# Performance work log

Hardware: AMD Instinct MI355X
Metric: run time of the kernel (lower is better)

## Reference

```python
import jax, jax.numpy as jnp
import numpy as np

B, NNODE, FIN, FOUT = 64, 512, 64, 64

def setup_inputs() -> dict:
    key = jax.random.key(0)
    ks = jax.random.split(key, 8)
    stdW = 1.0 / np.sqrt(FIN)
    stdA = 1.0 / np.sqrt(FOUT)
    return {
        "X": jax.random.normal(ks[0], (B, NNODE, FIN), dtype=jnp.float32),
        "A": jax.random.uniform(ks[1], (B, NNODE, NNODE), dtype=jnp.float32),
        "N": jax.random.randint(ks[2], (B,), 1, NNODE + 1, dtype=jnp.int64),
        "W": jax.random.uniform(ks[3], (FIN, FOUT), jnp.float32, -stdW, stdW),
        "a": jax.random.uniform(ks[4], (FOUT, FOUT), jnp.float32, -stdA, stdA),
        "bias_W": jax.random.uniform(ks[5], (FOUT,), jnp.float32, -stdW, stdW),
        "bias_a": jax.random.uniform(ks[6], (NNODE,), jnp.float32, -1.0 / np.sqrt(NNODE), 1.0 / np.sqrt(NNODE)),
    }

def reference(X, A, N, W, a, bias_W, bias_a):
    # A_ = A + identity on the top-left n_atoms block (only diagonal entries)
    idx = jnp.arange(A.shape[1])
    diag_mask = (idx[None, :] < N[:, None]).astype(A.dtype)  # [B, n]
    A_ = A + jnp.einsum('bn,nm->bnm', diag_mask, jnp.eye(A.shape[1], dtype=A.dtype))
    # XW: [B, n, F_out]
    XW = jnp.einsum('bnc,cd->bnd', X, W)
    # buf[a,j,k] = sum_i a[i,j] * XW^T[a,j,k]  (einsum 'ij,ajk->ajk')
    col_sum = a.sum(axis=0)  # [F_out]
    XWT = jnp.swapaxes(XW, 1, 2)  # [B, F_out, n]
    buf = col_sum[None, :, None] * XWT
    Z = jnp.einsum('bif,bfk->bik', XW, buf) + bias_a  # [B, n, n] + [n] broadcast on last dim
    att = jnp.tanh(jnp.einsum('bij,bjk->bik', A_, Z))
    H = jnp.einsum('bij,bjd->bid', att, XW) + bias_W
    return H
```

## Files before the change

### kernel.cpp

```cpp
#include <hip/hip_runtime.h>

#define BB 64
#define NN 512
#define FD 64

typedef short bf16x8 __attribute__((ext_vector_type(8)));
typedef float f32x4 __attribute__((ext_vector_type(4)));

__device__ __forceinline__ unsigned short f2bf(float f){
    unsigned u = __builtin_bit_cast(unsigned, f);
    u += 0x7fffu + ((u >> 16) & 1u);
    return (unsigned short)(u >> 16);
}
__device__ __forceinline__ float bf2f(unsigned short h){
    unsigned u = ((unsigned)h) << 16;
    return __builtin_bit_cast(float, u);
}
__device__ __forceinline__ float fast_tanh(float x){
    float e = __expf(2.0f * x);
    return 1.0f - 2.0f * __builtin_amdgcn_rcpf(e + 1.0f);
}

__global__ __launch_bounds__(256) void k_prep(const float* __restrict__ W,
                                              const float* __restrict__ a,
                                              float* __restrict__ colsum,
                                              unsigned short* __restrict__ Wt){
    int t = threadIdx.x;
    if (t < 64){
        float s = 0.f;
        #pragma unroll
        for (int i = 0; i < 64; i++) s += a[i*64 + t];
        colsum[t] = s;
    }
    int e0 = t * 16;
    int d = e0 >> 6, c0 = e0 & 63;
    #pragma unroll
    for (int q = 0; q < 16; q++)
        Wt[e0 + q] = f2bf(W[(c0 + q)*64 + d]);
}

__global__ __launch_bounds__(256) void k_xw(const float* __restrict__ X,
                                            const unsigned short* __restrict__ Wt,
                                            const float* __restrict__ colsum,
                                            unsigned short* __restrict__ XWh,
                                            unsigned short* __restrict__ XWt,
                                            unsigned short* __restrict__ St){
    __shared__ unsigned short Xl[64][72];
    __shared__ unsigned short Wtl[64][72];
    __shared__ unsigned short Cl[64][72];
    __shared__ float csl[64];
    int t = threadIdx.x;
    int row0 = blockIdx.x * 64;
    int r = t >> 2, c0 = (t & 3) * 16;
    {
        const float4* src = (const float4*)&X[(row0 + r)*FD + c0];
        #pragma unroll
        for (int q = 0; q < 4; q++){
            float4 v = src[q];
            ushort4 h; h.x=f2bf(v.x); h.y=f2bf(v.y); h.z=f2bf(v.z); h.w=f2bf(v.w);
            *(ushort4*)&Xl[r][c0 + q*4] = h;
        }
    }
    {
        const uint4* src = (const uint4*)&Wt[r*64 + c0];
        *(uint4*)&Wtl[r][c0]     = src[0];
        *(uint4*)&Wtl[r][c0 + 8] = src[1];
    }
    if (t < 64) csl[t] = colsum[t];
    __syncthreads();

    int lane = t & 63, w = t >> 6, l15 = lane & 15, quad = lane >> 4;
    f32x4 acc[4] = {{0,0,0,0},{0,0,0,0},{0,0,0,0},{0,0,0,0}};
    #pragma unroll
    for (int ks = 0; ks < 2; ks++){
        bf16x8 af = *(const bf16x8*)&Xl[w*16 + l15][ks*32 + quad*8];
        #pragma unroll
        for (int nt = 0; nt < 4; nt++){
            bf16x8 bfr = *(const bf16x8*)&Wtl[nt*16 + l15][ks*32 + quad*8];
            acc[nt] = __builtin_amdgcn_mfma_f32_16x16x32_bf16(af, bfr, acc[nt], 0, 0, 0);
        }
    }
    #pragma unroll
    for (int nt = 0; nt < 4; nt++)
        #pragma unroll
        for (int rg = 0; rg < 4; rg++)
            Cl[w*16 + quad*4 + rg][nt*16 + l15] = f2bf(acc[nt][rg]);
    __syncthreads();
    {
        uint4 v0 = *(const uint4*)&Cl[r][c0];
        uint4 v1 = *(const uint4*)&Cl[r][c0 + 8];
        *(uint4*)&XWh[(row0 + r)*FD + c0]     = v0;
        *(uint4*)&XWh[(row0 + r)*FD + c0 + 8] = v1;
    }
    {
        int b = blockIdx.x >> 3;
        int n0 = (blockIdx.x & 7) * 64;
        int f = r;
        float cs = csl[f];
        ushort4 hv[4], sv[4];
        #pragma unroll
        for (int q = 0; q < 4; q++)
            #pragma unroll
            for (int jj = 0; jj < 4; jj++){
                unsigned short hb = Cl[c0 + q*4 + jj][f];
                ((unsigned short*)&hv[q])[jj] = hb;
                ((unsigned short*)&sv[q])[jj] = f2bf(bf2f(hb) * cs);
            }
        unsigned short* dstT = &XWt[(b*64 + f)*NN + n0 + c0];
        unsigned short* dstS = &St [(b*64 + f)*NN + n0 + c0];
        #pragma unroll
        for (int q = 0; q < 4; q++){
            *(ushort4*)&dstT[q*4] = hv[q];
            *(ushort4*)&dstS[q*4] = sv[q];
        }
    }
}

__global__ __launch_bounds__(256) void k_m(const float* __restrict__ A,
                                           const unsigned short* __restrict__ St,
                                           const int* __restrict__ Ni,
                                           unsigned short* __restrict__ Mh,
                                           float* __restrict__ rowsum){
    __shared__ unsigned short Al[64][72];
    __shared__ unsigned short Sl[64][72];
    __shared__ float rsl[64][4];
    int t = threadIdx.x;
    int b = blockIdx.y, it = blockIdx.x;
    int i0 = it * 64;
    int Nb = (Ni[1] == 0) ? Ni[2*b] : Ni[b];
    int r = t >> 2, c0 = (t & 3) * 16;
    int lane = t & 63, w = t >> 6, l15 = lane & 15, quad = lane >> 4;
    f32x4 acc[4] = {{0,0,0,0},{0,0,0,0},{0,0,0,0},{0,0,0,0}};
    float rs = 0.f;
    const float* Ab = A + (b*NN + i0)*NN;
    for (int c = 0; c < 8; c++){
        __syncthreads();
        const float4* src = (const float4*)&Ab[r*NN + c*64 + c0];
        #pragma unroll
        for (int q = 0; q < 4; q++){
            float4 v = src[q];
            rs += v.x + v.y + v.z + v.w;
            ushort4 h; h.x=f2bf(v.x); h.y=f2bf(v.y); h.z=f2bf(v.z); h.w=f2bf(v.w);
            *(ushort4*)&Al[r][c0 + q*4] = h;
        }
        const uint4* s2 = (const uint4*)&St[(b*64 + r)*NN + c*64 + c0];
        *(uint4*)&Sl[r][c0]     = s2[0];
        *(uint4*)&Sl[r][c0 + 8] = s2[1];
        __syncthreads();
        #pragma unroll
        for (int ks = 0; ks < 2; ks++){
            bf16x8 af = *(const bf16x8*)&Al[w*16 + l15][ks*32 + quad*8];
            #pragma unroll
            for (int nt = 0; nt < 4; nt++){
                bf16x8 bfr = *(const bf16x8*)&Sl[nt*16 + l15][ks*32 + quad*8];
                acc[nt] = __builtin_amdgcn_mfma_f32_16x16x32_bf16(af, bfr, acc[nt], 0, 0, 0);
            }
        }
        if (c == it){
            #pragma unroll
            for (int nt = 0; nt < 4; nt++)
                #pragma unroll
                for (int rg = 0; rg < 4; rg++){
                    int iloc = w*16 + quad*4 + rg;
                    if (i0 + iloc < Nb)
                        acc[nt][rg] += bf2f(Sl[nt*16 + l15][iloc]);
                }
        }
    }
    rsl[r][t & 3] = rs;
    __syncthreads();
    #pragma unroll
    for (int nt = 0; nt < 4; nt++)
        #pragma unroll
        for (int rg = 0; rg < 4; rg++)
            Al[w*16 + quad*4 + rg][nt*16 + l15] = f2bf(acc[nt][rg]);
    __syncthreads();
    {
        uint4 v0 = *(const uint4*)&Al[r][c0];
        uint4 v1 = *(const uint4*)&Al[r][c0 + 8];
        *(uint4*)&Mh[(b*NN + i0 + r)*FD + c0]     = v0;
        *(uint4*)&Mh[(b*NN + i0 + r)*FD + c0 + 8] = v1;
    }
    if (t < 64){
        float s = rsl[t][0] + rsl[t][1] + rsl[t][2] + rsl[t][3];
        if (i0 + t < Nb) s += 1.f;
        rowsum[b*NN + i0 + t] = s;
    }
}

__global__ __launch_bounds__(256) void k_att(const unsigned short* __restrict__ Mh,
                                             const float* __restrict__ rowsum,
                                             const unsigned short* __restrict__ XWh,
                                             const unsigned short* __restrict__ XWt,
                                             const float* __restrict__ bias_a,
                                             const float* __restrict__ bias_W,
                                             float* __restrict__ H){
    __shared__ unsigned short Ml[64][72];
    __shared__ unsigned short Pl[64][72];
    __shared__ unsigned short XWl[64][72];
    __shared__ unsigned short XWtl[64][72];
    __shared__ float rsl[64];
    __shared__ float bl[64];
    int t = threadIdx.x;
    int b = blockIdx.y, it = blockIdx.x;
    int i0 = it * 64;
    int r = t >> 2, c0 = (t & 3) * 16;
    int lane = t & 63, w = t >> 6, l15 = lane & 15, quad = lane >> 4;
    {
        const uint4* src = (const uint4*)&Mh[(b*NN + i0 + r)*FD + c0];
        *(uint4*)&Ml[r][c0]     = src[0];
        *(uint4*)&Ml[r][c0 + 8] = src[1];
    }
    if (t < 64) rsl[t] = rowsum[b*NN + i0 + t];
    __syncthreads();
    bf16x8 maf[2];
    maf[0] = *(const bf16x8*)&Ml[w*16 + l15][quad*8];
    maf[1] = *(const bf16x8*)&Ml[w*16 + l15][32 + quad*8];
    float rs_r[4];
    #pragma unroll
    for (int rg = 0; rg < 4; rg++) rs_r[rg] = rsl[w*16 + quad*4 + rg];
    f32x4 hacc[4] = {{0,0,0,0},{0,0,0,0},{0,0,0,0},{0,0,0,0}};
    for (int jt = 0; jt < 8; jt++){
        __syncthreads();
        const uint4* s1 = (const uint4*)&XWh[(b*NN + jt*64 + r)*FD + c0];
        *(uint4*)&XWl[r][c0]     = s1[0];
        *(uint4*)&XWl[r][c0 + 8] = s1[1];
        const uint4* s2 = (const uint4*)&XWt[(b*64 + r)*NN + jt*64 + c0];
        *(uint4*)&XWtl[r][c0]     = s2[0];
        *(uint4*)&XWtl[r][c0 + 8] = s2[1];
        if (t < 64) bl[t] = bias_a[jt*64 + t];
        __syncthreads();
        #pragma unroll
        for (int nt = 0; nt < 4; nt++){
            float bv = bl[nt*16 + l15];
            f32x4 arg = { rs_r[0]*bv, rs_r[1]*bv, rs_r[2]*bv, rs_r[3]*bv };
            #pragma unroll
            for (int ks = 0; ks < 2; ks++){
                bf16x8 bfr = *(const bf16x8*)&XWl[nt*16 + l15][ks*32 + quad*8];
                arg = __builtin_amdgcn_mfma_f32_16x16x32_bf16(maf[ks], bfr, arg, 0, 0, 0);
            }
            #pragma unroll
            for (int rg = 0; rg < 4; rg++)
                Pl[w*16 + quad*4 + rg][nt*16 + l15] = f2bf(fast_tanh(arg[rg]));
        }
        __syncthreads();
        #pragma unroll
        for (int ks = 0; ks < 2; ks++){
            bf16x8 paf = *(const bf16x8*)&Pl[w*16 + l15][ks*32 + quad*8];
            #pragma unroll
            for (int dt = 0; dt < 4; dt++){
                bf16x8 bfr = *(const bf16x8*)&XWtl[dt*16 + l15][ks*32 + quad*8];
                hacc[dt] = __builtin_amdgcn_mfma_f32_16x16x32_bf16(paf, bfr, hacc[dt], 0, 0, 0);
            }
        }
    }
    #pragma unroll
    for (int dt = 0; dt < 4; dt++){
        float bw = bias_W[dt*16 + l15];
        #pragma unroll
        for (int rg = 0; rg < 4; rg++)
            H[(b*NN + i0 + w*16 + quad*4 + rg)*FD + dt*16 + l15] = hacc[dt][rg] + bw;
    }
}

extern "C" void kernel_launch(void* const* d_in, const int* in_sizes, int n_in,
                              void* d_out, int out_size, void* d_ws, size_t ws_size,
                              hipStream_t stream){
    const float* X      = (const float*)d_in[0];
    const float* A      = (const float*)d_in[1];
    const int*   N      = (const int*)  d_in[2];
    const float* W      = (const float*)d_in[3];
    const float* a      = (const float*)d_in[4];
    const float* bias_W = (const float*)d_in[5];
    const float* bias_a = (const float*)d_in[6];
    float* H = (float*)d_out;
    char* ws = (char*)d_ws;

    unsigned short* XWh = (unsigned short*)(ws);
    unsigned short* XWt = (unsigned short*)(ws + (4u<<20));
    unsigned short* St  = (unsigned short*)(ws + (8u<<20));
    unsigned short* Mh  = (unsigned short*)(ws + (12u<<20));
    float*          rowsum = (float*)(ws + (16u<<20));
    unsigned short* Wt     = (unsigned short*)(ws + (16u<<20) + 131072);
    float*          colsum = (float*)(ws + (16u<<20) + 139264);

    k_prep<<<1, 256, 0, stream>>>(W, a, colsum, Wt);
    k_xw  <<<BB * NN / 64, 256, 0, stream>>>(X, Wt, colsum, XWh, XWt, St);
    k_m   <<<dim3(8, BB), 256, 0, stream>>>(A, St, N, Mh, rowsum);
    k_att <<<dim3(8, BB), 256, 0, stream>>>(Mh, rowsum, XWh, XWt, bias_a, bias_W, H);
}
```

Measured before the change: 147.1 us.

## Fuse M and attention kernels, drop St buffer, prefetch tiles into registers

Merges the A·S product kernel and the attention kernel into one, so the intermediate M and rowsum stay in shared memory and never go to global memory. The column-sum scaling moves from a separate St buffer onto the M accumulator, which removes one global write and read pass. Both main loops now prefetch the next tile into registers while the current one is computed, and k_prep is parallelised with coalesced loads. The cost is more register and LDS use per block, which may reduce occupancy, and a small rounding change from scaling after the product instead of before.

```diff
diff --git a/kernel.cpp b/kernel.cpp
--- a/kernel.cpp
+++ b/kernel.cpp
@@ -25,30 +25,39 @@
                                               const float* __restrict__ a,
                                               float* __restrict__ colsum,
                                               unsigned short* __restrict__ Wt){
+    __shared__ float Wl[64][68];
+    __shared__ float cpart[4][64];
     int t = threadIdx.x;
-    if (t < 64){
-        float s = 0.f;
-        #pragma unroll
-        for (int i = 0; i < 64; i++) s += a[i*64 + t];
-        colsum[t] = s;
-    }
-    int e0 = t * 16;
-    int d = e0 >> 6, c0 = e0 & 63;
-    #pragma unroll
-    for (int q = 0; q < 16; q++)
-        Wt[e0 + q] = f2bf(W[(c0 + q)*64 + d]);
+    int d = t & 63, part = t >> 6;
+    float s = 0.f;
+    #pragma unroll
+    for (int i = 0; i < 16; i++) s += a[(part*16 + i)*64 + d];
+    cpart[part][d] = s;
+    int r = t >> 2, c0 = (t & 3) * 16;
+    {
+        const float4* src = (const float4*)&W[r*64 + c0];
+        #pragma unroll
+        for (int q = 0; q < 4; q++) *(float4*)&Wl[r][c0 + q*4] = src[q];
+    }
+    __syncthreads();
+    if (part == 0) colsum[d] = cpart[0][d] + cpart[1][d] + cpart[2][d] + cpart[3][d];
+    #pragma unroll
+    for (int q = 0; q < 4; q++){
+        ushort4 o;
+        #pragma unroll
+        for (int jj = 0; jj < 4; jj++)
+            ((unsigned short*)&o)[jj] = f2bf(Wl[c0 + q*4 + jj][r]);
+        *(ushort4*)&Wt[r*64 + c0 + q*4] = o;
+    }
 }
 
 __global__ __launch_bounds__(256) void k_xw(const float* __restrict__ X,
                                             const unsigned short* __restrict__ Wt,
-                                            const float* __restrict__ colsum,
                                             unsigned short* __restrict__ XWh,
-                                            unsigned short* __restrict__ XWt,
-                                            unsigned short* __restrict__ St){
+                                            unsigned short* __restrict__ XWt){
     __shared__ unsigned short Xl[64][72];
     __shared__ unsigned short Wtl[64][72];
     __shared__ unsigned short Cl[64][72];
-    __shared__ float csl[64];
     int t = threadIdx.x;
     int row0 = blockIdx.x * 64;
     int r = t >> 2, c0 = (t & 3) * 16;
@@ -60,15 +69,11 @@
             ushort4 h; h.x=f2bf(v.x); h.y=f2bf(v.y); h.z=f2bf(v.z); h.w=f2bf(v.w);
             *(ushort4*)&Xl[r][c0 + q*4] = h;
         }
-    }
-    {
-        const uint4* src = (const uint4*)&Wt[r*64 + c0];
-        *(uint4*)&Wtl[r][c0]     = src[0];
-        *(uint4*)&Wtl[r][c0 + 8] = src[1];
-    }
-    if (t < 64) csl[t] = colsum[t];
-    __syncthreads();
-
+        const uint4* src2 = (const uint4*)&Wt[r*64 + c0];
+        *(uint4*)&Wtl[r][c0]     = src2[0];
+        *(uint4*)&Wtl[r][c0 + 8] = src2[1];
+    }
+    __syncthreads();
     int lane = t & 63, w = t >> 6, l15 = lane & 15, quad = lane >> 4;
     f32x4 acc[4] = {{0,0,0,0},{0,0,0,0},{0,0,0,0},{0,0,0,0}};
     #pragma unroll
@@ -79,6 +84,14 @@
             bf16x8 bfr = *(const bf16x8*)&Wtl[nt*16 + l15][ks*32 + quad*8];
             acc[nt] = __builtin_amdgcn_mfma_f32_16x16x32_bf16(af, bfr, acc[nt], 0, 0, 0);
         }
+    }
+    int b = blockIdx.x >> 3, n0 = (blockIdx.x & 7) * 64;
+    #pragma unroll
+    for (int nt = 0; nt < 4; nt++){
+        ushort4 hv;
+        #pragma unroll
+        for (int rg = 0; rg < 4; rg++) ((unsigned short*)&hv)[rg] = f2bf(acc[nt][rg]);
+        *(ushort4*)&XWt[(b*64 + nt*16 + l15)*NN + n0 + w*16 + quad*4] = hv;
     }
     #pragma unroll
     for (int nt = 0; nt < 4; nt++)
@@ -92,67 +105,68 @@
         *(uint4*)&XWh[(row0 + r)*FD + c0]     = v0;
         *(uint4*)&XWh[(row0 + r)*FD + c0 + 8] = v1;
     }
-    {
-        int b = blockIdx.x >> 3;
-        int n0 = (blockIdx.x & 7) * 64;
-        int f = r;
-        float cs = csl[f];
-        ushort4 hv[4], sv[4];
-        #pragma unroll
-        for (int q = 0; q < 4; q++)
-            #pragma unroll
-            for (int jj = 0; jj < 4; jj++){
-                unsigned short hb = Cl[c0 + q*4 + jj][f];
-                ((unsigned short*)&hv[q])[jj] = hb;
-                ((unsigned short*)&sv[q])[jj] = f2bf(bf2f(hb) * cs);
-            }
-        unsigned short* dstT = &XWt[(b*64 + f)*NN + n0 + c0];
-        unsigned short* dstS = &St [(b*64 + f)*NN + n0 + c0];
-        #pragma unroll
-        for (int q = 0; q < 4; q++){
-            *(ushort4*)&dstT[q*4] = hv[q];
-            *(ushort4*)&dstS[q*4] = sv[q];
-        }
-    }
-}
-
-__global__ __launch_bounds__(256) void k_m(const float* __restrict__ A,
-                                           const unsigned short* __restrict__ St,
-                                           const int* __restrict__ Ni,
-                                           unsigned short* __restrict__ Mh,
-                                           float* __restrict__ rowsum){
-    __shared__ unsigned short Al[64][72];
-    __shared__ unsigned short Sl[64][72];
-    __shared__ float rsl[64][4];
+}
+
+__global__ __launch_bounds__(256) void k_fused(const float* __restrict__ A,
+                                               const unsigned short* __restrict__ XWh,
+                                               const unsigned short* __restrict__ XWt,
+                                               const float* __restrict__ colsum,
+                                               const int* __restrict__ Ni,
+                                               const float* __restrict__ bias_a,
+                                               const float* __restrict__ bias_W,
+                                               float* __restrict__ H){
+    __shared__ unsigned short s0[64][72];
+    __shared__ unsigned short s1[64][72];
+    __shared__ unsigned short Ml[64][72];
+    __shared__ unsigned short Pl[64][72];
+    __shared__ float rspart[64][4];
+    __shared__ float rsl[64];
+    __shared__ float csl[64];
+    __shared__ float bl[64];
     int t = threadIdx.x;
     int b = blockIdx.y, it = blockIdx.x;
     int i0 = it * 64;
     int Nb = (Ni[1] == 0) ? Ni[2*b] : Ni[b];
     int r = t >> 2, c0 = (t & 3) * 16;
     int lane = t & 63, w = t >> 6, l15 = lane & 15, quad = lane >> 4;
+    if (t < 64) csl[t] = colsum[t];
+    const float* Ab = A + (b*NN + i0)*NN;
+
+    float4 pA[4]; uint4 pB[2];
+    {
+        const float4* src = (const float4*)&Ab[r*NN + c0];
+        #pragma unroll
+        for (int q = 0; q < 4; q++) pA[q] = src[q];
+        const uint4* s2 = (const uint4*)&XWt[(b*64 + r)*NN + c0];
+        pB[0] = s2[0]; pB[1] = s2[1];
+    }
     f32x4 acc[4] = {{0,0,0,0},{0,0,0,0},{0,0,0,0},{0,0,0,0}};
     float rs = 0.f;
-    const float* Ab = A + (b*NN + i0)*NN;
     for (int c = 0; c < 8; c++){
         __syncthreads();
-        const float4* src = (const float4*)&Ab[r*NN + c*64 + c0];
         #pragma unroll
         for (int q = 0; q < 4; q++){
-            float4 v = src[q];
+            float4 v = pA[q];
             rs += v.x + v.y + v.z + v.w;
             ushort4 h; h.x=f2bf(v.x); h.y=f2bf(v.y); h.z=f2bf(v.z); h.w=f2bf(v.w);
-            *(ushort4*)&Al[r][c0 + q*4] = h;
-        }
-        const uint4* s2 = (const uint4*)&St[(b*64 + r)*NN + c*64 + c0];
-        *(uint4*)&Sl[r][c0]     = s2[0];
-        *(uint4*)&Sl[r][c0 + 8] = s2[1];
-        __syncthreads();
+            *(ushort4*)&s0[r][c0 + q*4] = h;
+        }
+        *(uint4*)&s1[r][c0]     = pB[0];
+        *(uint4*)&s1[r][c0 + 8] = pB[1];
+        __syncthreads();
+        if (c < 7){
+            const float4* src = (const float4*)&Ab[r*NN + (c+1)*64 + c0];
+            #pragma unroll
+            for (int q = 0; q < 4; q++) pA[q] = src[q];
+            const uint4* s2 = (const uint4*)&XWt[(b*64 + r)*NN + (c+1)*64 + c0];
+            pB[0] = s2[0]; pB[1] = s2[1];
+        }
         #pragma unroll
         for (int ks = 0; ks < 2; ks++){
-            bf16x8 af = *(const bf16x8*)&Al[w*16 + l15][ks*32 + quad*8];
+            bf16x8 af = *(const bf16x8*)&s0[w*16 + l15][ks*32 + quad*8];
             #pragma unroll
             for (int nt = 0; nt < 4; nt++){
-                bf16x8 bfr = *(const bf16x8*)&Sl[nt*16 + l15][ks*32 + quad*8];
+                bf16x8 bfr = *(const bf16x8*)&s1[nt*16 + l15][ks*32 + quad*8];
                 acc[nt] = __builtin_amdgcn_mfma_f32_16x16x32_bf16(af, bfr, acc[nt], 0, 0, 0);
             }
         }
@@ -163,55 +177,24 @@
                 for (int rg = 0; rg < 4; rg++){
                     int iloc = w*16 + quad*4 + rg;
                     if (i0 + iloc < Nb)
-                        acc[nt][rg] += bf2f(Sl[nt*16 + l15][iloc]);
+                        acc[nt][rg] += bf2f(s1[nt*16 + l15][iloc]);
                 }
         }
     }
-    rsl[r][t & 3] = rs;
-    __syncthreads();
-    #pragma unroll
-    for (int nt = 0; nt < 4; nt++)
+    rspart[r][t & 3] = rs;
+    #pragma unroll
+    for (int nt = 0; nt < 4; nt++){
+        float cs = csl[nt*16 + l15];
         #pragma unroll
         for (int rg = 0; rg < 4; rg++)
-            Al[w*16 + quad*4 + rg][nt*16 + l15] = f2bf(acc[nt][rg]);
-    __syncthreads();
-    {
-        uint4 v0 = *(const uint4*)&Al[r][c0];
-        uint4 v1 = *(const uint4*)&Al[r][c0 + 8];
-        *(uint4*)&Mh[(b*NN + i0 + r)*FD + c0]     = v0;
-        *(uint4*)&Mh[(b*NN + i0 + r)*FD + c0 + 8] = v1;
-    }
+            Ml[w*16 + quad*4 + rg][nt*16 + l15] = f2bf(acc[nt][rg] * cs);
+    }
+    __syncthreads();
     if (t < 64){
-        float s = rsl[t][0] + rsl[t][1] + rsl[t][2] + rsl[t][3];
+        float s = rspart[t][0] + rspart[t][1] + rspart[t][2] + rspart[t][3];
         if (i0 + t < Nb) s += 1.f;
-        rowsum[b*NN + i0 + t] = s;
-    }
-}
-
-__global__ __launch_bounds__(256) void k_att(const unsigned short* __restrict__ Mh,
-                                             const float* __restrict__ rowsum,
-                                             const unsigned short* __restrict__ XWh,
-                                             const unsigned short* __restrict__ XWt,
-                                             const float* __restrict__ bias_a,
-                                             const float* __restrict__ bias_W,
-                                             float* __restrict__ H){
-    __shared__ unsigned short Ml[64][72];
-    __shared__ unsigned short Pl[64][72];
-    __shared__ unsigned short XWl[64][72];
-    __shared__ unsigned short XWtl[64][72];
-    __shared__ float rsl[64];
-    __shared__ float bl[64];
-    int t = threadIdx.x;
-    int b = blockIdx.y, it = blockIdx.x;
-    int i0 = it * 64;
-    int r = t >> 2, c0 = (t & 3) * 16;
-    int lane = t & 63, w = t >> 6, l15 = lane & 15, quad = lane >> 4;
-    {
-        const uint4* src = (const uint4*)&Mh[(b*NN + i0 + r)*FD + c0];
-        *(uint4*)&Ml[r][c0]     = src[0];
-        *(uint4*)&Ml[r][c0 + 8] = src[1];
-    }
-    if (t < 64) rsl[t] = rowsum[b*NN + i0 + t];
+        rsl[t] = s;
+    }
     __syncthreads();
     bf16x8 maf[2];
     maf[0] = *(const bf16x8*)&Ml[w*16 + l15][quad*8];
@@ -219,24 +202,36 @@
     float rs_r[4];
     #pragma unroll
     for (int rg = 0; rg < 4; rg++) rs_r[rg] = rsl[w*16 + quad*4 + rg];
+
+    uint4 q1[2], q2[2];
+    {
+        const uint4* a1 = (const uint4*)&XWh[(b*NN + r)*FD + c0];
+        q1[0] = a1[0]; q1[1] = a1[1];
+        const uint4* a2 = (const uint4*)&XWt[(b*64 + r)*NN + c0];
+        q2[0] = a2[0]; q2[1] = a2[1];
+    }
     f32x4 hacc[4] = {{0,0,0,0},{0,0,0,0},{0,0,0,0},{0,0,0,0}};
     for (int jt = 0; jt < 8; jt++){
         __syncthreads();
-        const uint4* s1 = (const uint4*)&XWh[(b*NN + jt*64 + r)*FD + c0];
-        *(uint4*)&XWl[r][c0]     = s1[0];
-        *(uint4*)&XWl[r][c0 + 8] = s1[1];
-        const uint4* s2 = (const uint4*)&XWt[(b*64 + r)*NN + jt*64 + c0];
-        *(uint4*)&XWtl[r][c0]     = s2[0];
-        *(uint4*)&XWtl[r][c0 + 8] = s2[1];
+        *(uint4*)&s0[r][c0]     = q1[0];
+        *(uint4*)&s0[r][c0 + 8] = q1[1];
+        *(uint4*)&s1[r][c0]     = q2[0];
+        *(uint4*)&s1[r][c0 + 8] = q2[1];
         if (t < 64) bl[t] = bias_a[jt*64 + t];
         __syncthreads();
+        if (jt < 7){
+            const uint4* a1 = (const uint4*)&XWh[(b*NN + (jt+1)*64 + r)*FD + c0];
+            q1[0] = a1[0]; q1[1] = a1[1];
+            const uint4* a2 = (const uint4*)&XWt[(b*64 + r)*NN + (jt+1)*64 + c0];
+            q2[0] = a2[0]; q2[1] = a2[1];
+        }
         #pragma unroll
         for (int nt = 0; nt < 4; nt++){
             float bv = bl[nt*16 + l15];
             f32x4 arg = { rs_r[0]*bv, rs_r[1]*bv, rs_r[2]*bv, rs_r[3]*bv };
             #pragma unroll
             for (int ks = 0; ks < 2; ks++){
-                bf16x8 bfr = *(const bf16x8*)&XWl[nt*16 + l15][ks*32 + quad*8];
+                bf16x8 bfr = *(const bf16x8*)&s0[nt*16 + l15][ks*32 + quad*8];
                 arg = __builtin_amdgcn_mfma_f32_16x16x32_bf16(maf[ks], bfr, arg, 0, 0, 0);
             }
             #pragma unroll
@@ -249,7 +244,7 @@
             bf16x8 paf = *(const bf16x8*)&Pl[w*16 + l15][ks*32 + quad*8];
             #pragma unroll
             for (int dt = 0; dt < 4; dt++){
-                bf16x8 bfr = *(const bf16x8*)&XWtl[dt*16 + l15][ks*32 + quad*8];
+                bf16x8 bfr = *(const bf16x8*)&s1[dt*16 + l15][ks*32 + quad*8];
                 hacc[dt] = __builtin_amdgcn_mfma_f32_16x16x32_bf16(paf, bfr, hacc[dt], 0, 0, 0);
             }
         }
@@ -276,16 +271,12 @@
     float* H = (float*)d_out;
     char* ws = (char*)d_ws;
 
-    unsigned short* XWh = (unsigned short*)(ws);
-    unsigned short* XWt = (unsigned short*)(ws + (4u<<20));
-    unsigned short* St  = (unsigned short*)(ws + (8u<<20));
-    unsigned short* Mh  = (unsigned short*)(ws + (12u<<20));
-    float*          rowsum = (float*)(ws + (16u<<20));
-    unsigned short* Wt     = (unsigned short*)(ws + (16u<<20) + 131072);
-    float*          colsum = (float*)(ws + (16u<<20) + 139264);
-
-    k_prep<<<1, 256, 0, stream>>>(W, a, colsum, Wt);
-    k_xw  <<<BB * NN / 64, 256, 0, stream>>>(X, Wt, colsum, XWh, XWt, St);
-    k_m   <<<dim3(8, BB), 256, 0, stream>>>(A, St, N, Mh, rowsum);
-    k_att <<<dim3(8, BB), 256, 0, stream>>>(Mh, rowsum, XWh, XWt, bias_a, bias_W, H);
-}
+    unsigned short* XWh    = (unsigned short*)(ws);
+    unsigned short* XWt    = (unsigned short*)(ws + (4u<<20));
+    unsigned short* Wt     = (unsigned short*)(ws + (8u<<20));
+    float*          colsum = (float*)(ws + (8u<<20) + 8192);
+
+    k_prep <<<1, 256, 0, stream>>>(W, a, colsum, Wt);
+    k_xw   <<<BB * NN / 64, 256, 0, stream>>>(X, Wt, XWh, XWt);
+    k_fused<<<dim3(8, BB), 256, 0, stream>>>(A, XWh, XWt, colsum, N, bias_a, bias_W, H);
+}
```

Measured after the change: 151.7 us. 1.03x slower.
